# Kernel optimization log

Measured on AMD Instinct MI355X. Metric: run time of the kernel, lower is better.

The kernel has to match this reference:

```python
import jax, jax.numpy as jnp
import numpy as np

D = 1024          # hidden_dim
H = 16            # num_heads
G = 32            # number of graphs in the batch
N = 512           # nodes per graph (equal-size graphs -> the per-graph loop becomes one batched attention)
T = G * N         # total nodes
EPS = 1e-5


def _layernorm(x, g, b):
    mu = jnp.mean(x, axis=-1, keepdims=True)
    var = jnp.mean(jnp.square(x - mu), axis=-1, keepdims=True)
    return (x - mu) * jax.lax.rsqrt(var + EPS) * g + b


def setup_inputs() -> dict:
    key = jax.random.key(0)
    ks = jax.random.split(key, 10)
    s = 0.02
    inp = {
        "h": jax.random.normal(ks[0], (T, D), dtype=jnp.float32),
        "w_in": jax.random.normal(ks[1], (3 * D, D), dtype=jnp.float32) * s,   # MHA in_proj_weight
        "b_in": jnp.zeros((3 * D,), dtype=jnp.float32),
        "w_out": jax.random.normal(ks[2], (D, D), dtype=jnp.float32) * s,      # MHA out_proj
        "b_out": jnp.zeros((D,), dtype=jnp.float32),
        "ln1_g": jnp.ones((D,), dtype=jnp.float32),
        "ln1_b": jnp.zeros((D,), dtype=jnp.float32),
        "ln2_g": jnp.ones((D,), dtype=jnp.float32),
        "ln2_b": jnp.zeros((D,), dtype=jnp.float32),
        "ffn_w1": jax.random.normal(ks[3], (2 * D, D), dtype=jnp.float32) * s,
        "ffn_b1": jnp.zeros((2 * D,), dtype=jnp.float32),
        "ffn_w2": jax.random.normal(ks[4], (D, 2 * D), dtype=jnp.float32) * s,
        "ffn_b2": jnp.zeros((D,), dtype=jnp.float32),
        "edge_index": jax.random.randint(ks[5], (2, 65536), 0, T, dtype=jnp.int64),
        "batch": jnp.repeat(jnp.arange(G, dtype=jnp.int64), N),
        "num_graphs": G,
    }
    return inp


def reference(h, w_in, b_in, w_out, b_out, ln1_g, ln1_b, ln2_g, ln2_b,
              ffn_w1, ffn_b1, ffn_w2, ffn_b2, edge_index, batch, num_graphs):
    # Per-graph self-attention: equal-size contiguous graphs -> reshape to [G, N, D]
    hd = D // H
    x = h.reshape(num_graphs, -1, D)                       # [G, N, D]
    n = x.shape[1]
    qkv = x @ w_in.T + b_in                                # [G, N, 3D]
    q, k, v = jnp.split(qkv, 3, axis=-1)
    q = q.reshape(num_graphs, n, H, hd).transpose(0, 2, 1, 3)  # [G, H, N, hd]
    k = k.reshape(num_graphs, n, H, hd).transpose(0, 2, 1, 3)
    v = v.reshape(num_graphs, n, H, hd).transpose(0, 2, 1, 3)
    scores = jnp.einsum('ghnd,ghmd->ghnm', q, k) / np.sqrt(hd)
    attn = jax.nn.softmax(scores, axis=-1)
    o = jnp.einsum('ghnm,ghmd->ghnd', attn, v)             # [G, H, N, hd]
    o = o.transpose(0, 2, 1, 3).reshape(num_graphs, n, D)
    o = o @ w_out.T + b_out
    x = _layernorm(x + o, ln1_g, ln1_b)                    # residual + norm1
    f = jax.nn.relu(x @ ffn_w1.T + ffn_b1) @ ffn_w2.T + ffn_b2  # dropout: eval mode (identity)
    x = _layernorm(x + f, ln2_g, ln2_b)                    # residual + norm2
    return x.reshape(-1, D)                                # [T, D]
```

## Files before the change

### kernel.cpp

```cpp
#include <hip/hip_runtime.h>
#include <stdint.h>

typedef unsigned short u16;
typedef __attribute__((ext_vector_type(8))) short bf16x8;
typedef __attribute__((ext_vector_type(4))) float f32x4;

#define AS1C(p) ((const __attribute__((address_space(1))) char*)(const char*)(p))
#define AS3C(p) ((__attribute__((address_space(3))) char*)(char*)(p))

static __device__ __forceinline__ u16 f2bf(float f) {
  uint32_t u = __builtin_bit_cast(uint32_t, f);
  u = (u + 0x7FFFu + ((u >> 16) & 1u)) >> 16;
  return (u16)u;
}

__global__ __launch_bounds__(256) void k_f2bf(const float* __restrict__ src,
                                              u16* __restrict__ dst, int n4) {
  int i = blockIdx.x * blockDim.x + threadIdx.x;
  if (i >= n4) return;
  float4 v = reinterpret_cast<const float4*>(src)[i];
  ushort4 o;
  o.x = f2bf(v.x); o.y = f2bf(v.y); o.z = f2bf(v.z); o.w = f2bf(v.w);
  reinterpret_cast<ushort4*>(dst)[i] = o;
}

template<bool OUT_BF16, bool RELU>
__global__ __launch_bounds__(512, 2) void k_gemm256(const u16* __restrict__ A,
                                                    const u16* __restrict__ B,
                                                    const float* __restrict__ bias,
                                                    void* __restrict__ C,
                                                    int M, int N, int K) {
  __shared__ __align__(16) char lds[98304];
  const int tid = threadIdx.x, lane = tid & 63, wid = tid >> 6;
  const int wm = wid >> 2, wn = wid & 3;

  const int nbx = N >> 8;
  const int cpx = gridDim.x >> 3;
  const int sid = ((int)blockIdx.x & 7) * cpx + ((int)blockIdx.x >> 3);
  const int bm = (sid / nbx) << 8;
  const int bn = (sid % nbx) << 8;

  int ga[2], gb[2];
  unsigned wdst[2];
#pragma unroll
  for (int c = 0; c < 2; ++c) {
    const int o = wid * 2048 + c * 1024 + lane * 16;
    const int r = o >> 6;
    const int kb = (((o >> 4) & 3) ^ (r & 3)) * 16;
    ga[c] = (bm + r) * K * 2 + kb;
    gb[c] = (bn + r) * K * 2 + kb;
    wdst[c] = (unsigned)__builtin_amdgcn_readfirstlane(wid * 2048 + c * 1024);
  }
  const char* Ag = (const char*)A;
  const char* Bg = (const char*)B;

  const int arow = wm * 128 + (lane & 15);
  const int brow = wn * 64 + (lane & 15);
  const int ckA = ((lane >> 4) ^ (arow & 3)) * 16;
  const int ckB = ((lane >> 4) ^ (brow & 3)) * 16;

  f32x4 acc[8][4];
#pragma unroll
  for (int m = 0; m < 8; ++m)
#pragma unroll
    for (int n = 0; n < 4; ++n) acc[m][n] = 0.f;
  bf16x8 am[8], bfr[4];

#define STG(t, b) do { \
  const int koff_ = (t) * 64; \
  _Pragma("unroll") for (int c_ = 0; c_ < 2; ++c_) { \
    __builtin_amdgcn_global_load_lds(AS1C(Ag + ga[c_] + koff_), \
        AS3C(lds + ((b) * 32768 + wdst[c_])), 16, 0, 0); \
    __builtin_amdgcn_global_load_lds(AS1C(Bg + gb[c_] + koff_), \
        AS3C(lds + ((b) * 32768 + 16384 + wdst[c_])), 16, 0, 0); \
  } } while (0)

#define MM(mh) do { \
  __builtin_amdgcn_s_setprio(1); \
  _Pragma("unroll") for (int m_ = 0; m_ < 4; ++m_) \
  _Pragma("unroll") for (int n_ = 0; n_ < 4; ++n_) \
    acc[(mh) * 4 + m_][n_] = __builtin_amdgcn_mfma_f32_16x16x32_bf16( \
        am[(mh) * 4 + m_], bfr[n_], acc[(mh) * 4 + m_][n_], 0, 0, 0); \
  __builtin_amdgcn_s_setprio(0); } while (0)

  const int nT = K >> 5, tmask = nT - 1;

  STG(0, 0); STG(1, 1);
  asm volatile("s_waitcnt vmcnt(4)" ::: "memory");
  __builtin_amdgcn_sched_barrier(0);
  __builtin_amdgcn_s_barrier();

  int bR = 0;
  for (int t = 0; t < nT; ++t) {
    const int bW = (bR >= 1) ? bR - 1 : 2;
    const int base = bR * 32768;
#pragma unroll
    for (int m_ = 0; m_ < 4; ++m_)
      am[m_] = *(const bf16x8*)(lds + base + (arow + m_ * 16) * 64 + ckA);
#pragma unroll
    for (int n_ = 0; n_ < 4; ++n_)
      bfr[n_] = *(const bf16x8*)(lds + base + 16384 + (brow + n_ * 16) * 64 + ckB);
#pragma unroll
    for (int m_ = 4; m_ < 8; ++m_)
      am[m_] = *(const bf16x8*)(lds + base + (arow + m_ * 16) * 64 + ckA);
    STG((t + 2) & tmask, bW);
    asm volatile("s_waitcnt lgkmcnt(4)" ::: "memory");
    __builtin_amdgcn_sched_barrier(0);
    MM(0);
    asm volatile("s_waitcnt lgkmcnt(0)" ::: "memory");
    __builtin_amdgcn_sched_barrier(0);
    MM(1);
    asm volatile("s_waitcnt vmcnt(4)" ::: "memory");
    __builtin_amdgcn_sched_barrier(0);
    __builtin_amdgcn_s_barrier();
    bR = (bR == 2) ? 0 : bR + 1;
  }
  asm volatile("s_waitcnt vmcnt(0)" ::: "memory");

  u16* Cb = (u16*)C;
  float* Cf = (float*)C;
#pragma unroll
  for (int n = 0; n < 4; ++n) {
    const int col = bn + wn * 64 + n * 16 + (lane & 15);
    const float bv = bias[col];
#pragma unroll
    for (int m = 0; m < 8; ++m) {
      const int rbase = bm + wm * 128 + m * 16 + (lane >> 4) * 4;
#pragma unroll
      for (int q = 0; q < 4; ++q) {
        float v = acc[m][n][q] + bv;
        if (RELU) v = fmaxf(v, 0.f);
        const long idx = (long)(rbase + q) * N + col;
        if (OUT_BF16) Cb[idx] = f2bf(v);
        else          Cf[idx] = v;
      }
    }
  }
#undef STG
#undef MM
}

__global__ __launch_bounds__(256) void k_transpose_v(const u16* __restrict__ qkv,
                                                     u16* __restrict__ vt) {
  const int gh = blockIdx.x, g = gh >> 4, h = gh & 15;
  const int tid = threadIdx.x;
  __shared__ __align__(16) u16 tile[4096];
  for (int nt = 0; nt < 8; ++nt) {
    const int n0 = nt * 64;
#pragma unroll
    for (int c = 0; c < 2; ++c) {
      const int ch = tid * 2 + c;
      const int n = ch >> 3;
      const int cc = ch & 7;
      const uint4 v = *reinterpret_cast<const uint4*>(
          qkv + (long)(g * 512 + n0 + n) * 3072 + 2048 + h * 64 + cc * 8);
      const int phys = cc ^ (n & 7) ^ (n >> 3);
      *reinterpret_cast<uint4*>(tile + n * 64 + phys * 8) = v;
    }
    __syncthreads();
#pragma unroll
    for (int c = 0; c < 2; ++c) {
      const int ch = tid * 2 + c;
      const int crow = ch >> 3;
      const int noff = (ch & 7) * 8;
      union { u16 s[8]; uint4 u; } val;
#pragma unroll
      for (int i = 0; i < 8; ++i) {
        const int n = noff + i;
        const int phys = (crow >> 3) ^ (n & 7) ^ (n >> 3);
        val.s[i] = tile[n * 64 + phys * 8 + (crow & 7)];
      }
      *reinterpret_cast<uint4*>(vt + (long)(gh * 64 + crow) * 512 + n0 + noff) = val.u;
    }
    __syncthreads();
  }
}

__global__ __launch_bounds__(256) void k_attn(const u16* __restrict__ qkv,
                                              const u16* __restrict__ vt,
                                              u16* __restrict__ out) {
  __shared__ __align__(16) char Ks[8192];
  __shared__ __align__(16) char Vs[8192];
  __shared__ __align__(16) char Ps[4][2048];
  const int tid = threadIdx.x, lane = tid & 63, wid = tid >> 6;
  const int qb = blockIdx.x, h = blockIdx.y, g = blockIdx.z;
  const int gh = g * 16 + h;
  const long grow0 = (long)g * 512;
  const char* qbase = (const char*)qkv;

  const long qrow = qb * 64 + wid * 16 + (lane & 15);
  bf16x8 qf[2];
#pragma unroll
  for (int kf = 0; kf < 2; ++kf) {
    const long go = (((grow0 + qrow) * 3072) + h * 64 + kf * 32 + (lane >> 4) * 8) * 2;
    qf[kf] = *reinterpret_cast<const bf16x8*>(qbase + go);
  }

  f32x4 oacc[4];
#pragma unroll
  for (int i = 0; i < 4; i++) oacc[i] = 0.f;
  float mrun[4], lrun[4];
#pragma unroll
  for (int q = 0; q < 4; q++) { mrun[q] = -3.0e38f; lrun[q] = 0.f; }

  const unsigned l0 = (unsigned)__builtin_amdgcn_readfirstlane(wid * 2048);
  const unsigned l1 = l0 + 1024;

  for (int it = 0; it < 8; ++it) {
    const int kv0 = it * 64;
#pragma unroll
    for (int c = 0; c < 2; ++c) {
      const int o = wid * 2048 + c * 1024 + lane * 16;
      const int row = o >> 7;
      const int pch = (o >> 4) & 7;
      const int lch = pch ^ (row & 7);
      const long gK = (((grow0 + kv0 + row) * 3072) + 1024 + h * 64 + lch * 8) * 2;
      __builtin_amdgcn_global_load_lds(AS1C(qbase + gK), AS3C(Ks + (c ? l1 : l0)), 16, 0, 0);
      const long gV = (((long)(gh * 64 + row)) * 512 + kv0 + lch * 8) * 2;
      __builtin_amdgcn_global_load_lds(AS1C((const char*)vt + gV), AS3C(Vs + (c ? l1 : l0)), 16, 0, 0);
    }
    __syncthreads();

    f32x4 s[4];
#pragma unroll
    for (int nt = 0; nt < 4; ++nt) {
      const int krow = nt * 16 + (lane & 15);
      const int sw = krow & 7;
      const bf16x8 k0 = *reinterpret_cast<const bf16x8*>(Ks + krow * 128 + (((lane >> 4)) ^ sw) * 16);
      const bf16x8 k1 = *reinterpret_cast<const bf16x8*>(Ks + krow * 128 + (((lane >> 4) + 4) ^ sw) * 16);
      f32x4 t = 0.f;
      t = __builtin_amdgcn_mfma_f32_16x16x32_bf16(qf[0], k0, t, 0, 0, 0);
      t = __builtin_amdgcn_mfma_f32_16x16x32_bf16(qf[1], k1, t, 0, 0, 0);
#pragma unroll
      for (int q = 0; q < 4; q++) t[q] *= 0.125f;
      s[nt] = t;
    }

    float tmax[4];
#pragma unroll
    for (int q = 0; q < 4; q++)
      tmax[q] = fmaxf(fmaxf(s[0][q], s[1][q]), fmaxf(s[2][q], s[3][q]));
#pragma unroll
    for (int d = 1; d < 16; d <<= 1)
#pragma unroll
      for (int q = 0; q < 4; q++) tmax[q] = fmaxf(tmax[q], __shfl_xor(tmax[q], d));
    float sf[4];
#pragma unroll
    for (int q = 0; q < 4; q++) {
      const float mn = fmaxf(mrun[q], tmax[q]);
      sf[q] = __expf(mrun[q] - mn);
      mrun[q] = mn;
    }
    float rs[4] = {0.f, 0.f, 0.f, 0.f};
#pragma unroll
    for (int nt = 0; nt < 4; nt++)
#pragma unroll
      for (int q = 0; q < 4; q++) {
        const float p = __expf(s[nt][q] - mrun[q]);
        s[nt][q] = p;
        rs[q] += p;
      }
#pragma unroll
    for (int d = 1; d < 16; d <<= 1)
#pragma unroll
      for (int q = 0; q < 4; q++) rs[q] += __shfl_xor(rs[q], d);
#pragma unroll
    for (int q = 0; q < 4; q++) lrun[q] = lrun[q] * sf[q] + rs[q];
#pragma unroll
    for (int i = 0; i < 4; i++)
#pragma unroll
      for (int q = 0; q < 4; q++) oacc[i][q] *= sf[q];

    char* pw = Ps[wid];
#pragma unroll
    for (int nt = 0; nt < 4; nt++) {
      const int cc = nt * 16 + (lane & 15);
#pragma unroll
      for (int q = 0; q < 4; q++) {
        const int r = (lane >> 4) * 4 + q;
        const int phys = (cc >> 3) ^ (r & 7);
        *(u16*)(pw + r * 128 + phys * 16 + (cc & 7) * 2) = f2bf(s[nt][q]);
      }
    }

#pragma unroll
    for (int kf = 0; kf < 2; ++kf) {
      const int prow = lane & 15;
      const bf16x8 pa = *reinterpret_cast<const bf16x8*>(
          pw + prow * 128 + ((kf * 4 + (lane >> 4)) ^ (prow & 7)) * 16);
#pragma unroll
      for (int ot = 0; ot < 4; ++ot) {
        const int vr = ot * 16 + (lane & 15);
        const bf16x8 vb = *reinterpret_cast<const bf16x8*>(
            Vs + vr * 128 + ((kf * 4 + (lane >> 4)) ^ (vr & 7)) * 16);
        oacc[ot] = __builtin_amdgcn_mfma_f32_16x16x32_bf16(pa, vb, oacc[ot], 0, 0, 0);
      }
    }
    __syncthreads();
  }

#pragma unroll
  for (int ot = 0; ot < 4; ++ot) {
    const int col = h * 64 + ot * 16 + (lane & 15);
#pragma unroll
    for (int q = 0; q < 4; q++) {
      const long r = grow0 + qb * 64 + wid * 16 + (lane >> 4) * 4 + q;
      out[r * 1024 + col] = f2bf(oacc[ot][q] / lrun[q]);
    }
  }
}

template<bool EMIT_BF16>
__global__ __launch_bounds__(256) void k_ln(const float* __restrict__ A,
                                            const float* __restrict__ Bz,
                                            const float* __restrict__ gam,
                                            const float* __restrict__ bet,
                                            float* __restrict__ out_f,
                                            u16* __restrict__ out_b) {
  const int row = blockIdx.x;
  const int tid = threadIdx.x;
  const long base = (long)row * 1024;
  const float4 a = reinterpret_cast<const float4*>(A + base)[tid];
  const float4 b = reinterpret_cast<const float4*>(Bz + base)[tid];
  const float x0 = a.x + b.x, x1 = a.y + b.y, x2 = a.z + b.z, x3 = a.w + b.w;
  float s1 = x0 + x1 + x2 + x3;
  float s2 = x0 * x0 + x1 * x1 + x2 * x2 + x3 * x3;
#pragma unroll
  for (int d = 1; d < 64; d <<= 1) { s1 += __shfl_xor(s1, d); s2 += __shfl_xor(s2, d); }
  __shared__ float red[8];
  const int wid = tid >> 6, lane = tid & 63;
  if (lane == 0) { red[wid] = s1; red[4 + wid] = s2; }
  __syncthreads();
  s1 = red[0] + red[1] + red[2] + red[3];
  s2 = red[4] + red[5] + red[6] + red[7];
  const float mu = s1 * (1.f / 1024.f);
  const float var = s2 * (1.f / 1024.f) - mu * mu;
  const float rstd = rsqrtf(var + 1e-5f);
  const float4 gv = reinterpret_cast<const float4*>(gam)[tid];
  const float4 bv = reinterpret_cast<const float4*>(bet)[tid];
  float4 y;
  y.x = (x0 - mu) * rstd * gv.x + bv.x;
  y.y = (x1 - mu) * rstd * gv.y + bv.y;
  y.z = (x2 - mu) * rstd * gv.z + bv.z;
  y.w = (x3 - mu) * rstd * gv.w + bv.w;
  reinterpret_cast<float4*>(out_f + base)[tid] = y;
  if (EMIT_BF16) {
    ushort4 o;
    o.x = f2bf(y.x); o.y = f2bf(y.y); o.z = f2bf(y.z); o.w = f2bf(y.w);
    reinterpret_cast<ushort4*>(out_b + base)[tid] = o;
  }
}

extern "C" void kernel_launch(void* const* d_in, const int* in_sizes, int n_in,
                              void* d_out, int out_size, void* d_ws, size_t ws_size,
                              hipStream_t stream) {
  const float* h    = (const float*)d_in[0];
  const float* w_in = (const float*)d_in[1];
  const float* b_in = (const float*)d_in[2];
  const float* w_o  = (const float*)d_in[3];
  const float* b_o  = (const float*)d_in[4];
  const float* ln1g = (const float*)d_in[5];
  const float* ln1b = (const float*)d_in[6];
  const float* ln2g = (const float*)d_in[7];
  const float* ln2b = (const float*)d_in[8];
  const float* w1   = (const float*)d_in[9];
  const float* b1   = (const float*)d_in[10];
  const float* w2   = (const float*)d_in[11];
  const float* b2   = (const float*)d_in[12];

  const size_t WS_NEED = 184549376;
  if (ws_size < WS_NEED) {
    hipMemsetAsync(d_out, 0, (size_t)out_size * 4, stream);
    return;
  }

  char* W = (char*)d_ws;
  u16* h_bf     = (u16*)(W + 0);
  u16* w_in_bf  = (u16*)(W + 33554432);
  u16* w_out_bf = (u16*)(W + 39845888);
  u16* w1_bf    = (u16*)(W + 41943040);
  u16* w2_bf    = (u16*)(W + 46137344);
  u16* qkv      = (u16*)(W + 50331648);
  u16* vt       = (u16*)(W + 150994944);
  float* x1     = (float*)(W + 50331648);
  u16* f1       = (u16*)(W + 117440512);
  u16* attn_bf  = h_bf;
  u16* x1_bf    = h_bf;
  float* o32    = (float*)d_out;
  float* f2     = (float*)d_out;

  k_f2bf<<<dim3(16384), 256, 0, stream>>>(h, h_bf, 4194304);
  k_f2bf<<<dim3(3072),  256, 0, stream>>>(w_in, w_in_bf, 786432);
  k_f2bf<<<dim3(1024),  256, 0, stream>>>(w_o, w_out_bf, 262144);
  k_f2bf<<<dim3(2048),  256, 0, stream>>>(w1, w1_bf, 524288);
  k_f2bf<<<dim3(2048),  256, 0, stream>>>(w2, w2_bf, 524288);

  k_gemm256<true, false><<<dim3(768), 512, 0, stream>>>(h_bf, w_in_bf, b_in, (void*)qkv, 16384, 3072, 1024);
  k_transpose_v<<<dim3(512), 256, 0, stream>>>(qkv, vt);
  k_attn<<<dim3(8, 16, 32), 256, 0, stream>>>(qkv, vt, attn_bf);
  k_gemm256<false, false><<<dim3(256), 512, 0, stream>>>(attn_bf, w_out_bf, b_o, (void*)o32, 16384, 1024, 1024);
  k_ln<true><<<dim3(16384), 256, 0, stream>>>(h, o32, ln1g, ln1b, x1, x1_bf);
  k_gemm256<true, true><<<dim3(512), 512, 0, stream>>>(x1_bf, w1_bf, b1, (void*)f1, 16384, 2048, 1024);
  k_gemm256<false, false><<<dim3(256), 512, 0, stream>>>(f1, w2_bf, b2, (void*)f2, 16384, 1024, 2048);
  k_ln<false><<<dim3(16384), 256, 0, stream>>>(x1, f2, ln2g, ln2b, (float*)d_out, (u16*)nullptr);
}
```

Before: 685.1 us.

## Double-buffer attention K/V loads, fuse bf16 casts, reswizzle GEMM LDS

Merges the five fp32-to-bf16 conversion launches into one kernel that picks its source and destination from the block index. Changes the GEMM LDS XOR swizzle to also mix higher row bits, aiming to cut bank conflicts on fragment reads. Reorders the GEMM epilogue so adjacent column stores sit together, with the bias values preloaded. Double-buffers the K/V tiles in the attention kernel so the next tile's global-to-LDS load overlaps the current tile's compute. This doubles the attention kernel's K/V LDS footprint and replaces two __syncthreads per iteration with one explicit waitcnt plus barrier.

```diff
diff --git a/kernel.cpp b/kernel.cpp
--- a/kernel.cpp
+++ b/kernel.cpp
@@ -14,14 +14,22 @@
   return (u16)u;
 }
 
-__global__ __launch_bounds__(256) void k_f2bf(const float* __restrict__ src,
-                                              u16* __restrict__ dst, int n4) {
-  int i = blockIdx.x * blockDim.x + threadIdx.x;
-  if (i >= n4) return;
-  float4 v = reinterpret_cast<const float4*>(src)[i];
+__global__ __launch_bounds__(256) void k_f2bf5(const float* __restrict__ s0, u16* __restrict__ d0,
+                                               const float* __restrict__ s1, u16* __restrict__ d1,
+                                               const float* __restrict__ s2, u16* __restrict__ d2,
+                                               const float* __restrict__ s3, u16* __restrict__ d3,
+                                               const float* __restrict__ s4, u16* __restrict__ d4) {
+  const int bid = blockIdx.x;
+  const float* s; u16* d; int i;
+  if (bid < 16384)      { s = s0; d = d0; i = bid * 256 + threadIdx.x; }
+  else if (bid < 19456) { s = s1; d = d1; i = (bid - 16384) * 256 + threadIdx.x; }
+  else if (bid < 20480) { s = s2; d = d2; i = (bid - 19456) * 256 + threadIdx.x; }
+  else if (bid < 22528) { s = s3; d = d3; i = (bid - 20480) * 256 + threadIdx.x; }
+  else                  { s = s4; d = d4; i = (bid - 22528) * 256 + threadIdx.x; }
+  float4 v = reinterpret_cast<const float4*>(s)[i];
   ushort4 o;
   o.x = f2bf(v.x); o.y = f2bf(v.y); o.z = f2bf(v.z); o.w = f2bf(v.w);
-  reinterpret_cast<ushort4*>(dst)[i] = o;
+  reinterpret_cast<ushort4*>(d)[i] = o;
 }
 
 template<bool OUT_BF16, bool RELU>
@@ -46,7 +54,8 @@
   for (int c = 0; c < 2; ++c) {
     const int o = wid * 2048 + c * 1024 + lane * 16;
     const int r = o >> 6;
-    const int kb = (((o >> 4) & 3) ^ (r & 3)) * 16;
+    const int c2 = (o >> 4) & 3;
+    const int kb = (c2 ^ (r & 3) ^ ((r >> 2) & 3)) * 16;
     ga[c] = (bm + r) * K * 2 + kb;
     gb[c] = (bn + r) * K * 2 + kb;
     wdst[c] = (unsigned)__builtin_amdgcn_readfirstlane(wid * 2048 + c * 1024);
@@ -56,8 +65,7 @@
 
   const int arow = wm * 128 + (lane & 15);
   const int brow = wn * 64 + (lane & 15);
-  const int ckA = ((lane >> 4) ^ (arow & 3)) * 16;
-  const int ckB = ((lane >> 4) ^ (brow & 3)) * 16;
+  const int ck = (((lane >> 4) ^ (lane & 3) ^ ((lane >> 2) & 3)) & 3) * 16;
 
   f32x4 acc[8][4];
 #pragma unroll
@@ -96,13 +104,13 @@
     const int base = bR * 32768;
 #pragma unroll
     for (int m_ = 0; m_ < 4; ++m_)
-      am[m_] = *(const bf16x8*)(lds + base + (arow + m_ * 16) * 64 + ckA);
+      am[m_] = *(const bf16x8*)(lds + base + (arow + m_ * 16) * 64 + ck);
 #pragma unroll
     for (int n_ = 0; n_ < 4; ++n_)
-      bfr[n_] = *(const bf16x8*)(lds + base + 16384 + (brow + n_ * 16) * 64 + ckB);
+      bfr[n_] = *(const bf16x8*)(lds + base + 16384 + (brow + n_ * 16) * 64 + ck);
 #pragma unroll
     for (int m_ = 4; m_ < 8; ++m_)
-      am[m_] = *(const bf16x8*)(lds + base + (arow + m_ * 16) * 64 + ckA);
+      am[m_] = *(const bf16x8*)(lds + base + (arow + m_ * 16) * 64 + ck);
     STG((t + 2) & tmask, bW);
     asm volatile("s_waitcnt lgkmcnt(4)" ::: "memory");
     __builtin_amdgcn_sched_barrier(0);
@@ -117,22 +125,23 @@
   }
   asm volatile("s_waitcnt vmcnt(0)" ::: "memory");
 
+  float bv[4];
+#pragma unroll
+  for (int n = 0; n < 4; ++n) bv[n] = bias[bn + wn * 64 + n * 16 + (lane & 15)];
   u16* Cb = (u16*)C;
   float* Cf = (float*)C;
 #pragma unroll
-  for (int n = 0; n < 4; ++n) {
-    const int col = bn + wn * 64 + n * 16 + (lane & 15);
-    const float bv = bias[col];
-#pragma unroll
-    for (int m = 0; m < 8; ++m) {
-      const int rbase = bm + wm * 128 + m * 16 + (lane >> 4) * 4;
-#pragma unroll
-      for (int q = 0; q < 4; ++q) {
-        float v = acc[m][n][q] + bv;
+  for (int m = 0; m < 8; ++m) {
+#pragma unroll
+    for (int q = 0; q < 4; ++q) {
+      const long row = bm + wm * 128 + m * 16 + (lane >> 4) * 4 + q;
+      const long basei = row * N + bn + wn * 64 + (lane & 15);
+#pragma unroll
+      for (int n = 0; n < 4; ++n) {
+        float v = acc[m][n][q] + bv[n];
         if (RELU) v = fmaxf(v, 0.f);
-        const long idx = (long)(rbase + q) * N + col;
-        if (OUT_BF16) Cb[idx] = f2bf(v);
-        else          Cf[idx] = v;
+        if (OUT_BF16) Cb[basei + n * 16] = f2bf(v);
+        else          Cf[basei + n * 16] = v;
       }
     }
   }
@@ -179,14 +188,14 @@
 __global__ __launch_bounds__(256) void k_attn(const u16* __restrict__ qkv,
                                               const u16* __restrict__ vt,
                                               u16* __restrict__ out) {
-  __shared__ __align__(16) char Ks[8192];
-  __shared__ __align__(16) char Vs[8192];
+  __shared__ __align__(16) char KV[2][16384];
   __shared__ __align__(16) char Ps[4][2048];
   const int tid = threadIdx.x, lane = tid & 63, wid = tid >> 6;
   const int qb = blockIdx.x, h = blockIdx.y, g = blockIdx.z;
   const int gh = g * 16 + h;
   const long grow0 = (long)g * 512;
   const char* qbase = (const char*)qkv;
+  const char* vbase = (const char*)vt;
 
   const long qrow = qb * 64 + wid * 16 + (lane & 15);
   bf16x8 qf[2];
@@ -196,6 +205,26 @@
     qf[kf] = *reinterpret_cast<const bf16x8*>(qbase + go);
   }
 
+  long gKb[2], gVb[2];
+  unsigned dK[2];
+#pragma unroll
+  for (int c = 0; c < 2; ++c) {
+    const int o = wid * 2048 + c * 1024 + lane * 16;
+    const int row = o >> 7;
+    const int lch = ((o >> 4) & 7) ^ (row & 7);
+    gKb[c] = (((grow0 + row) * 3072) + 1024 + h * 64 + lch * 8) * 2;
+    gVb[c] = (((long)(gh * 64 + row)) * 512 + lch * 8) * 2;
+    dK[c] = (unsigned)__builtin_amdgcn_readfirstlane(wid * 2048 + c * 1024);
+  }
+
+#define STGKV(kv0_, buf_) do { \
+  _Pragma("unroll") for (int c_ = 0; c_ < 2; ++c_) { \
+    __builtin_amdgcn_global_load_lds(AS1C(qbase + gKb[c_] + (long)(kv0_) * 6144), \
+        AS3C(&KV[buf_][0] + dK[c_]), 16, 0, 0); \
+    __builtin_amdgcn_global_load_lds(AS1C(vbase + gVb[c_] + (long)(kv0_) * 2), \
+        AS3C(&KV[buf_][0] + 8192 + dK[c_]), 16, 0, 0); \
+  } } while (0)
+
   f32x4 oacc[4];
 #pragma unroll
   for (int i = 0; i < 4; i++) oacc[i] = 0.f;
@@ -203,31 +232,25 @@
 #pragma unroll
   for (int q = 0; q < 4; q++) { mrun[q] = -3.0e38f; lrun[q] = 0.f; }
 
-  const unsigned l0 = (unsigned)__builtin_amdgcn_readfirstlane(wid * 2048);
-  const unsigned l1 = l0 + 1024;
+  STGKV(0, 0);
 
   for (int it = 0; it < 8; ++it) {
-    const int kv0 = it * 64;
-#pragma unroll
-    for (int c = 0; c < 2; ++c) {
-      const int o = wid * 2048 + c * 1024 + lane * 16;
-      const int row = o >> 7;
-      const int pch = (o >> 4) & 7;
-      const int lch = pch ^ (row & 7);
-      const long gK = (((grow0 + kv0 + row) * 3072) + 1024 + h * 64 + lch * 8) * 2;
-      __builtin_amdgcn_global_load_lds(AS1C(qbase + gK), AS3C(Ks + (c ? l1 : l0)), 16, 0, 0);
-      const long gV = (((long)(gh * 64 + row)) * 512 + kv0 + lch * 8) * 2;
-      __builtin_amdgcn_global_load_lds(AS1C((const char*)vt + gV), AS3C(Vs + (c ? l1 : l0)), 16, 0, 0);
-    }
-    __syncthreads();
+    const int buf = it & 1;
+    asm volatile("s_waitcnt vmcnt(0)" ::: "memory");
+    __builtin_amdgcn_sched_barrier(0);
+    __builtin_amdgcn_s_barrier();
+    __builtin_amdgcn_sched_barrier(0);
+    if (it < 7) STGKV(it * 64 + 64, buf ^ 1);
+    const char* Kb = &KV[buf][0];
+    const char* Vb = &KV[buf][0] + 8192;
 
     f32x4 s[4];
 #pragma unroll
     for (int nt = 0; nt < 4; ++nt) {
       const int krow = nt * 16 + (lane & 15);
       const int sw = krow & 7;
-      const bf16x8 k0 = *reinterpret_cast<const bf16x8*>(Ks + krow * 128 + (((lane >> 4)) ^ sw) * 16);
-      const bf16x8 k1 = *reinterpret_cast<const bf16x8*>(Ks + krow * 128 + (((lane >> 4) + 4) ^ sw) * 16);
+      const bf16x8 k0 = *reinterpret_cast<const bf16x8*>(Kb + krow * 128 + (((lane >> 4)) ^ sw) * 16);
+      const bf16x8 k1 = *reinterpret_cast<const bf16x8*>(Kb + krow * 128 + (((lane >> 4) + 4) ^ sw) * 16);
       f32x4 t = 0.f;
       t = __builtin_amdgcn_mfma_f32_16x16x32_bf16(qf[0], k0, t, 0, 0, 0);
       t = __builtin_amdgcn_mfma_f32_16x16x32_bf16(qf[1], k1, t, 0, 0, 0);
@@ -292,12 +315,12 @@
       for (int ot = 0; ot < 4; ++ot) {
         const int vr = ot * 16 + (lane & 15);
         const bf16x8 vb = *reinterpret_cast<const bf16x8*>(
-            Vs + vr * 128 + ((kf * 4 + (lane >> 4)) ^ (vr & 7)) * 16);
+            Vb + vr * 128 + ((kf * 4 + (lane >> 4)) ^ (vr & 7)) * 16);
         oacc[ot] = __builtin_amdgcn_mfma_f32_16x16x32_bf16(pa, vb, oacc[ot], 0, 0, 0);
       }
     }
-    __syncthreads();
-  }
+  }
+#undef STGKV
 
 #pragma unroll
   for (int ot = 0; ot < 4; ++ot) {
@@ -389,11 +412,8 @@
   float* o32    = (float*)d_out;
   float* f2     = (float*)d_out;
 
-  k_f2bf<<<dim3(16384), 256, 0, stream>>>(h, h_bf, 4194304);
-  k_f2bf<<<dim3(3072),  256, 0, stream>>>(w_in, w_in_bf, 786432);
-  k_f2bf<<<dim3(1024),  256, 0, stream>>>(w_o, w_out_bf, 262144);
-  k_f2bf<<<dim3(2048),  256, 0, stream>>>(w1, w1_bf, 524288);
-  k_f2bf<<<dim3(2048),  256, 0, stream>>>(w2, w2_bf, 524288);
+  k_f2bf5<<<dim3(24576), 256, 0, stream>>>(h, h_bf, w_in, w_in_bf, w_o, w_out_bf,
+                                           w1, w1_bf, w2, w2_bf);
 
   k_gemm256<true, false><<<dim3(768), 512, 0, stream>>>(h_bf, w_in_bf, b_in, (void*)qkv, 16384, 3072, 1024);
   k_transpose_v<<<dim3(512), 256, 0, stream>>>(qkv, vt);
```

Result: faster. 668.5 us (-2.4%).
